# Optimization experiments

Measured on AMD Instinct MI355X. Metric: run time of the kernel, lower is better.

Reference implementation:

```python
import jax, jax.numpy as jnp
import numpy as np

EMBED_DIM = 1024
NUM_HEADS = 16
HEAD_DIM = EMBED_DIM // NUM_HEADS


def setup_inputs() -> dict:
    key = jax.random.key(0)
    ks = jax.random.split(key, 9)
    B, S, E, hd = 2, 2048, EMBED_DIM, HEAD_DIM
    s_e = 1.0 / np.sqrt(E)
    return {
        "x": jax.random.normal(ks[0], (B, S, E), dtype=jnp.float32),
        "wq": jax.random.uniform(ks[1], (E, E), jnp.float32, -s_e, s_e),
        "bq": jax.random.uniform(ks[2], (E,), jnp.float32, -s_e, s_e),
        "wk": jax.random.uniform(ks[3], (E, hd), jnp.float32, -s_e, s_e),
        "bk": jax.random.uniform(ks[4], (hd,), jnp.float32, -s_e, s_e),
        "wv": jax.random.uniform(ks[5], (E, hd), jnp.float32, -s_e, s_e),
        "bv": jax.random.uniform(ks[6], (hd,), jnp.float32, -s_e, s_e),
        "wo": jax.random.uniform(ks[7], (E, E), jnp.float32, -s_e, s_e),
        "bo": jax.random.uniform(ks[8], (E,), jnp.float32, -s_e, s_e),
    }


def reference(x, wq, bq, wk, bk, wv, bv, wo, bo):
    B, S, E = x.shape
    H, hd = NUM_HEADS, HEAD_DIM
    # projections
    q = (x @ wq + bq).reshape(B, S, H, hd)          # [B,S,H,hd]
    k = x @ wk + bk                                  # [B,S,hd] shared across heads
    v = x @ wv + bv                                  # [B,S,hd]
    scale = 1.0 / np.sqrt(hd).astype(np.float32)
    # scores: [B,H,S_q,S_k]
    scores = jnp.einsum('bqhd,bkd->bhqk', q, k) * scale
    attn = jax.nn.softmax(scores, axis=-1)
    out = jnp.einsum('bhqk,bkd->bqhd', attn, v).reshape(B, S, E)
    return out @ wo + bo
```

## Files before the change

kernel.cpp:

```cpp
#include <hip/hip_runtime.h>
#include <stdint.h>

#define SLEN 2048
#define EDIM 1024
#define NH 16
#define HD 64
#define QLD 1152
#define NSPLIT 2

typedef unsigned short u16;
typedef short bf8 __attribute__((ext_vector_type(8)));
typedef float f4 __attribute__((ext_vector_type(4)));
typedef float f16f __attribute__((ext_vector_type(16)));
typedef int v2i __attribute__((ext_vector_type(2)));
typedef bf8 bf8_a __attribute__((may_alias));
typedef uint2 uint2_a __attribute__((may_alias));
typedef uint4 uint4_a __attribute__((may_alias));

__device__ __forceinline__ float bf2f(u16 u) {
  union { unsigned u; float f; } c; c.u = ((unsigned)u) << 16; return c.f;
}
__device__ __forceinline__ u16 f2bf(float x) {
  union { __bf16 h; u16 u; } c; c.h = (__bf16)x; return c.u;
}
__device__ __forceinline__ unsigned pk2bf(float a, float b) {
  union { __bf16 h[2]; unsigned u; } c;
  c.h[0] = (__bf16)a; c.h[1] = (__bf16)b;
  return c.u;
}
__device__ __forceinline__ void async_cp16(u16* lds, const u16* g) {
  __builtin_amdgcn_global_load_lds((__attribute__((address_space(1))) void*)g,
                                   (__attribute__((address_space(3))) void*)lds,
                                   16, 0, 0);
}

__device__ __forceinline__ void tcvt_tile(const float* src, int srcLd,
                                          u16* dst, int dstLd, int r0, int c0) {
  __shared__ u16 tile[64][65];
  const int t = threadIdx.x;
#pragma unroll
  for (int i = 0; i < 16; ++i) {
    int e = i * 256 + t, rr = e >> 6, cc = e & 63;
    tile[rr][cc] = f2bf(src[(size_t)(r0 + rr) * srcLd + c0 + cc]);
  }
  __syncthreads();
#pragma unroll
  for (int i = 0; i < 16; ++i) {
    int e = i * 256 + t, j = e >> 6, ii = e & 63;
    dst[(size_t)(c0 + j) * dstLd + r0 + ii] = tile[ii][j];
  }
}

__global__ void prep_w(const float* wq, const float* wk, const float* wv,
                       const float* wo, const float* bq, const float* bk,
                       const float* bv, const float* bo, const float* x,
                       u16* wT, u16* woT, float* bQKV, float* bOut, u16* xbf) {
  const int yy = blockIdx.y;
  if (yy < 16) tcvt_tile(wq, 1024, wT, 1024, blockIdx.x * 64, yy * 64);
  else if (yy < 32) tcvt_tile(wo, 1024, woT, 1024, blockIdx.x * 64, (yy - 16) * 64);
  else if (yy == 32) tcvt_tile(wk, 64, wT + (size_t)1024 * 1024, 1024, blockIdx.x * 64, 0);
  else if (yy == 33) tcvt_tile(wv, 64, wT + (size_t)1088 * 1024, 1024, blockIdx.x * 64, 0);
  else if (yy == 34) {
    int i = blockIdx.x * 256 + threadIdx.x;
    if (i < 1024) bQKV[i] = bq[i];
    else if (i < 1088) bQKV[i] = bk[i - 1024];
    else if (i < 1152) bQKV[i] = bv[i - 1088];
    int j = i - 1152;
    if (j >= 0 && j < 1024) bOut[j] = bo[j];
  } else {
    const int blk = (yy - 35) * 16 + blockIdx.x, t = threadIdx.x;
#pragma unroll
    for (int i = 0; i < 8; ++i) {
      int idx = blk * 16384 + i * 2048 + t * 8;
      u16 tmp[8];
#pragma unroll
      for (int j = 0; j < 8; ++j) tmp[j] = f2bf(x[idx + j]);
      *(uint4_a*)&xbf[idx] = *(const uint4_a*)tmp;
    }
  }
}

__global__ __launch_bounds__(256) void gemm_bt_bias(
    const u16* __restrict__ A, const u16* __restrict__ Bt,
    const float* __restrict__ bias, void* __restrict__ C, int K, int ldc,
    int ofp32, u16* __restrict__ vtb) {
  __shared__ __align__(16) u16 As[64 * 64];
  __shared__ __align__(16) u16 Bs[128 * 64];
  const int tn0 = blockIdx.x * 128, tm0 = blockIdx.y * 64;
  const int tid = threadIdx.x, wave = tid >> 6, lane = tid & 63;
  const int quad = lane >> 4, l16 = lane & 15;
  const int wm = wave & 1, wn = wave >> 1;

  f4 acc[2][4];
#pragma unroll
  for (int i = 0; i < 2; ++i)
#pragma unroll
    for (int j = 0; j < 4; ++j) acc[i][j] = f4{0.f, 0.f, 0.f, 0.f};

  int aslot[2], bslot[4]; size_t aoff[2], boff[4];
#pragma unroll
  for (int i = 0; i < 2; ++i) {
    int s = i * 256 + tid, m = s >> 3, kc = s & 7, c = (kc - m) & 7;
    aslot[i] = s; aoff[i] = (size_t)(tm0 + m) * K + c * 8;
  }
#pragma unroll
  for (int i = 0; i < 4; ++i) {
    int s = i * 256 + tid, n = s >> 3, kc = s & 7, c = (kc - n) & 7;
    bslot[i] = s; boff[i] = (size_t)(tn0 + n) * K + c * 8;
  }
  int ard[2][2], brd[4][2];
#pragma unroll
  for (int mi = 0; mi < 2; ++mi) {
    int m = wm * 32 + mi * 16 + l16;
#pragma unroll
    for (int kk = 0; kk < 2; ++kk)
      ard[mi][kk] = (m * 8 + (((kk * 4 + quad) + m) & 7)) * 8;
  }
#pragma unroll
  for (int ni = 0; ni < 4; ++ni) {
    int n = wn * 64 + ni * 16 + l16;
#pragma unroll
    for (int kk = 0; kk < 2; ++kk)
      brd[ni][kk] = (n * 8 + (((kk * 4 + quad) + n) & 7)) * 8;
  }

  const int kIt = K >> 6;
  for (int it = 0; it < kIt; ++it) {
    __syncthreads();
    const size_t kb = (size_t)it * 64;
#pragma unroll
    for (int i = 0; i < 2; ++i) async_cp16(&As[aslot[i] * 8], A + aoff[i] + kb);
#pragma unroll
    for (int i = 0; i < 4; ++i) async_cp16(&Bs[bslot[i] * 8], Bt + boff[i] + kb);
    __syncthreads();
#pragma unroll
    for (int kk = 0; kk < 2; ++kk) {
      bf8 af[2], bfr[4];
#pragma unroll
      for (int mi = 0; mi < 2; ++mi) af[mi] = *(const bf8_a*)&As[ard[mi][kk]];
#pragma unroll
      for (int ni = 0; ni < 4; ++ni) bfr[ni] = *(const bf8_a*)&Bs[brd[ni][kk]];
#pragma unroll
      for (int mi = 0; mi < 2; ++mi)
#pragma unroll
        for (int ni = 0; ni < 4; ++ni)
          acc[mi][ni] = __builtin_amdgcn_mfma_f32_16x16x32_bf16(
              af[mi], bfr[ni], acc[mi][ni], 0, 0, 0);
    }
  }

  const float QSCALE = 0.125f * 1.44269504089f;
  float bv[4];
#pragma unroll
  for (int ni = 0; ni < 4; ++ni) bv[ni] = bias[tn0 + wn * 64 + ni * 16 + l16];
#pragma unroll
  for (int mi = 0; mi < 2; ++mi) {
    int row0 = tm0 + wm * 32 + mi * 16 + quad * 4;
#pragma unroll
    for (int ni = 0; ni < 4; ++ni) {
      int col = tn0 + wn * 64 + ni * 16 + l16;
      float vv[4];
#pragma unroll
      for (int r = 0; r < 4; ++r) vv[r] = acc[mi][ni][r] + bv[ni];
      if (vtb != nullptr && col < 1024) {
#pragma unroll
        for (int r = 0; r < 4; ++r) vv[r] *= QSCALE;
      }
      if (ofp32) {
#pragma unroll
        for (int r = 0; r < 4; ++r)
          ((float*)C)[(size_t)(row0 + r) * ldc + col] = vv[r];
      } else {
#pragma unroll
        for (int r = 0; r < 4; ++r)
          ((u16*)C)[(size_t)(row0 + r) * ldc + col] = f2bf(vv[r]);
      }
      if (vtb != nullptr && col >= 1088) {
        int d = col - 1088, bb = row0 >> 11, s0 = row0 & 2047;
        uint2 pk;
        pk.x = pk2bf(vv[0], vv[1]);
        pk.y = pk2bf(vv[2], vv[3]);
        *(uint2_a*)&vtb[(size_t)(bb * 64 + d) * SLEN + s0] = pk;
      }
    }
  }
}

__global__ __launch_bounds__(256, 4) void attn_kernel(
    const u16* __restrict__ qkv, const u16* __restrict__ vT,
    u16* __restrict__ Opart, float* __restrict__ lpart) {
  __shared__ __align__(16) u16 Kf[2][4096];
  __shared__ __align__(16) u16 Vf[2][4096];
  const int qt = blockIdx.x, bh = blockIdx.y, ks = blockIdx.z;
  const int b = bh >> 4, h = bh & 15;
  const int tid = threadIdx.x, wave = tid >> 6, lane = tid & 63;
  const int l31 = lane & 31, hi = lane >> 5, r16l = lane & 15;
  const int base_k = (l31 >> 4) * 64 + hi * 16 + r16l;

  u16* Kflat = &Kf[0][0];
#pragma unroll
  for (int i = 0; i < 4; ++i) {
    int d = i * 256 + tid;
    int kk = d >> 9, g = (d >> 6) & 7, qd = (d >> 4) & 3, r16 = d & 15;
    async_cp16(&Kflat[d * 8],
               qkv + (size_t)(b * SLEN + qt * 128 + g * 16 + r16) * QLD +
                   h * HD + (kk * 4 + qd) * 8);
  }
  __syncthreads();
  bf8 bq[4];
#pragma unroll
  for (int kk2 = 0; kk2 < 4; ++kk2) {
    int c = base_k + wave * 128 + (kk2 >> 1) * 512 + (kk2 & 1) * 32;
    bq[kk2] = *(const bf8_a*)&Kflat[c * 8];
  }
  __syncthreads();

  const int kbase = ks * (SLEN / NSPLIT);
  const u16* kp[2]; const u16* vp[2];
#pragma unroll
  for (int i = 0; i < 2; ++i) {
    int d = i * 256 + tid;
    int kk = d >> 8, k8 = (d >> 6) & 3, qd = (d >> 4) & 3, r16 = d & 15;
    kp[i] = qkv + (size_t)(b * SLEN + kbase + k8 * 16 + r16) * QLD + EDIM +
            (kk * 4 + qd) * 8;
    int k4 = d >> 8, ni = (d >> 6) & 3;
    vp[i] = vT + (size_t)(b * 64 + ni * 16 + r16) * SLEN + kbase +
            (k4 * 4 + qd) * 8;
  }
  auto stage = [&](int bsel) {
#pragma unroll
    for (int i = 0; i < 2; ++i) {
      int d = i * 256 + tid;
      async_cp16(&Kf[bsel][d * 8], kp[i]);
      async_cp16(&Vf[bsel][d * 8], vp[i]);
      kp[i] += 64 * QLD;
      vp[i] += 64;
    }
  };
  stage(0);

  f16f acc_o[2];
#pragma unroll
  for (int i = 0; i < 2; ++i)
#pragma unroll
    for (int r = 0; r < 16; ++r) acc_o[i][r] = 0.f;
  f4 lracc = f4{0.f, 0.f, 0.f, 0.f};

  const int NHALF = SLEN / NSPLIT / 64;
  for (int hh = 0; hh < NHALF; ++hh) {
    __syncthreads();
    if (hh < NHALF - 1) stage((hh + 1) & 1);
    const int bsel = hh & 1;
    const u16* kf = &Kf[bsel][0];
    const u16* vf = &Vf[bsel][0];

    f16f st[2];
#pragma unroll
    for (int j = 0; j < 2; ++j)
#pragma unroll
      for (int r = 0; r < 16; ++r) st[j][r] = 0.f;
    __builtin_amdgcn_s_setprio(1);
#pragma unroll
    for (int kk2 = 0; kk2 < 4; ++kk2) {
#pragma unroll
      for (int j32 = 0; j32 < 2; ++j32) {
        bf8 ak = *(const bf8_a*)
            &kf[(base_k + (kk2 >> 1) * 256 + j32 * 128 + (kk2 & 1) * 32) * 8];
        st[j32] = __builtin_amdgcn_mfma_f32_32x32x16_bf16(ak, bq[kk2],
                                                          st[j32], 0, 0, 0);
      }
    }
    __builtin_amdgcn_s_setprio(0);

    bf8 pa[2][2];
#pragma unroll
    for (int j32 = 0; j32 < 2; ++j32) {
      float pe[16];
#pragma unroll
      for (int r = 0; r < 16; ++r) {
        pe[r] = __builtin_amdgcn_exp2f(st[j32][r]);
        lracc[r & 3] += pe[r];
      }
      int a0 = (int)pk2bf(pe[0], pe[1]),   b0 = (int)pk2bf(pe[4], pe[5]);
      int a1 = (int)pk2bf(pe[2], pe[3]),   b1 = (int)pk2bf(pe[6], pe[7]);
      int a2 = (int)pk2bf(pe[8], pe[9]),   b2 = (int)pk2bf(pe[12], pe[13]);
      int a3 = (int)pk2bf(pe[10], pe[11]), b3 = (int)pk2bf(pe[14], pe[15]);
      v2i s0 = __builtin_amdgcn_permlane32_swap(a0, b0, false, false);
      v2i s1 = __builtin_amdgcn_permlane32_swap(a1, b1, false, false);
      v2i s2 = __builtin_amdgcn_permlane32_swap(a2, b2, false, false);
      v2i s3 = __builtin_amdgcn_permlane32_swap(a3, b3, false, false);
      union { int i[4]; bf8 v; } up0, up1;
      up0.i[0] = s0[0]; up0.i[1] = s1[0]; up0.i[2] = s0[1]; up0.i[3] = s1[1];
      up1.i[0] = s2[0]; up1.i[1] = s3[0]; up1.i[2] = s2[1]; up1.i[3] = s3[1];
      pa[j32][0] = up0.v;
      pa[j32][1] = up1.v;
    }

    __builtin_amdgcn_s_setprio(1);
#pragma unroll
    for (int j32 = 0; j32 < 2; ++j32)
#pragma unroll
      for (int ks2 = 0; ks2 < 2; ++ks2)
#pragma unroll
        for (int ni2 = 0; ni2 < 2; ++ni2) {
          bf8 bv = *(const bf8_a*)
              &vf[(base_k + j32 * 256 + ni2 * 128 + ks2 * 32) * 8];
          acc_o[ni2] = __builtin_amdgcn_mfma_f32_32x32x16_bf16(
              pa[j32][ks2], bv, acc_o[ni2], 0, 0, 0);
        }
    __builtin_amdgcn_s_setprio(0);
  }

  const size_t pbase = (size_t)((ks * 32 + bh) * 16 + qt) * 128;
  float lr = (lracc[0] + lracc[1]) + (lracc[2] + lracc[3]);
  float s = lr + __shfl_xor(lr, 32, 64);
  if (lane < 32) lpart[pbase + wave * 32 + lane] = s;
#pragma unroll
  for (int ni2 = 0; ni2 < 2; ++ni2)
#pragma unroll
    for (int r = 0; r < 16; ++r) {
      int q = (r & 3) + 8 * (r >> 2) + 4 * hi;
      Opart[(pbase + wave * 32 + q) * 64 + ni2 * 32 + l31] =
          f2bf(acc_o[ni2][r]);
    }
}

__global__ __launch_bounds__(256) void reduce_o(const u16* __restrict__ Op,
                                                const float* __restrict__ lp,
                                                u16* __restrict__ aob) {
  const int qt = blockIdx.x, bh = blockIdx.y, b = bh >> 4, h = bh & 15;
  const int t = threadIdx.x, r = t >> 1, dh = (t & 1) * 32;
  size_t p[NSPLIT];
#pragma unroll
  for (int i = 0; i < NSPLIT; ++i)
    p[i] = (size_t)((i * 32 + bh) * 16 + qt) * 128;
  float lsum = 0.f;
#pragma unroll
  for (int i = 0; i < NSPLIT; ++i) lsum += lp[p[i] + r];
  const float inv = 1.f / lsum;
  u16* dst = aob + (size_t)(b * SLEN + qt * 128 + r) * EDIM + h * HD + dh;
#pragma unroll
  for (int c = 0; c < 4; ++c) {
    float accv[8] = {0.f, 0.f, 0.f, 0.f, 0.f, 0.f, 0.f, 0.f};
#pragma unroll
    for (int i = 0; i < NSPLIT; ++i) {
      uint4 a = *(const uint4_a*)(Op + (p[i] + r) * 64 + dh + c * 8);
      const u16* pa = (const u16*)&a;
#pragma unroll
      for (int j = 0; j < 8; ++j) accv[j] += bf2f(pa[j]);
    }
    u16 outv[8];
#pragma unroll
    for (int j = 0; j < 8; ++j) outv[j] = f2bf(accv[j] * inv);
    *(uint4_a*)(dst + c * 8) = *(const uint4_a*)outv;
  }
}

extern "C" void kernel_launch(void* const* d_in, const int* in_sizes, int n_in,
                              void* d_out, int out_size, void* d_ws, size_t ws_size,
                              hipStream_t stream) {
  const float* x  = (const float*)d_in[0];
  const float* wq = (const float*)d_in[1];
  const float* bq = (const float*)d_in[2];
  const float* wk = (const float*)d_in[3];
  const float* bk = (const float*)d_in[4];
  const float* wv = (const float*)d_in[5];
  const float* bv = (const float*)d_in[6];
  const float* wo = (const float*)d_in[7];
  const float* bo = (const float*)d_in[8];

  char* ws = (char*)d_ws;
  size_t off = 0;
  auto carve = [&](size_t bytes) {
    void* p = ws + off;
    off = (off + bytes + 255) & ~(size_t)255;
    return p;
  };
  u16* wT      = (u16*)carve((size_t)1152 * 1024 * 2);
  u16* woT     = (u16*)carve((size_t)1024 * 1024 * 2);
  float* bQKV  = (float*)carve(1152 * 4);
  float* bOut  = (float*)carve(1024 * 4);
  u16* xbf     = (u16*)carve((size_t)4096 * EDIM * 2);
  u16* qkvb    = (u16*)carve((size_t)4096 * QLD * 2);
  u16* vTb     = (u16*)carve((size_t)2 * 64 * SLEN * 2);
  u16* Opart   = (u16*)carve((size_t)NSPLIT * 32 * 16 * 128 * 64 * 2);
  float* lpart = (float*)carve((size_t)NSPLIT * 32 * 16 * 128 * 4);
  u16* aob     = (u16*)carve((size_t)4096 * EDIM * 2);

  prep_w<<<dim3(16, 51), 256, 0, stream>>>(wq, wk, wv, wo, bq, bk, bv, bo, x,
                                           wT, woT, bQKV, bOut, xbf);

  gemm_bt_bias<<<dim3(9, 64), 256, 0, stream>>>(xbf, wT, bQKV, qkvb, 1024, QLD,
                                                0, vTb);

  attn_kernel<<<dim3(16, 32, NSPLIT), 256, 0, stream>>>(qkvb, vTb, Opart, lpart);
  reduce_o<<<dim3(16, 32), 256, 0, stream>>>(Opart, lpart, aob);

  gemm_bt_bias<<<dim3(8, 64), 256, 0, stream>>>(aob, woT, bOut, d_out, 1024,
                                                1024, 1, nullptr);
}
```

Baseline: 182.3 us.

## Process 256 query rows per attention block to reuse K/V tiles

Each attention block now handles 256 queries instead of 128, with each wave holding two 32-query sets. Every K and V tile staged in shared memory is reused across twice as many MFMAs, which halves the K/V global and LDS traffic per query. In exchange the block uses roughly double the accumulator registers (launch bounds drop from 4 to 2 waves-per-SIMD hint) and the grid is half as many blocks (512 total), which may reduce occupancy and latency hiding. The reduce kernel indexing is updated to match the new partial layout.

Measured after the change: 178.1 us. 1.02x faster.

```diff
diff --git a/kernel.cpp b/kernel.cpp
--- a/kernel.cpp
+++ b/kernel.cpp
@@ -186,7 +186,7 @@
   }
 }
 
-__global__ __launch_bounds__(256, 4) void attn_kernel(
+__global__ __launch_bounds__(256, 2) void attn_kernel(
     const u16* __restrict__ qkv, const u16* __restrict__ vT,
     u16* __restrict__ Opart, float* __restrict__ lpart) {
   __shared__ __align__(16) u16 Kf[2][4096];
@@ -198,20 +198,30 @@
   const int base_k = (l31 >> 4) * 64 + hi * 16 + r16l;
 
   u16* Kflat = &Kf[0][0];
-#pragma unroll
-  for (int i = 0; i < 4; ++i) {
+  u16* Vflat = &Vf[0][0];
+#pragma unroll
+  for (int i = 0; i < 8; ++i) {
     int d = i * 256 + tid;
-    int kk = d >> 9, g = (d >> 6) & 7, qd = (d >> 4) & 3, r16 = d & 15;
-    async_cp16(&Kflat[d * 8],
-               qkv + (size_t)(b * SLEN + qt * 128 + g * 16 + r16) * QLD +
+    int sel = d >> 10, dl = d & 1023;
+    int kk = dl >> 9, g = (dl >> 6) & 7, qd = (dl >> 4) & 3, r16 = dl & 15;
+    u16* dstf = sel ? Vflat : Kflat;
+    async_cp16(&dstf[dl * 8],
+               qkv + (size_t)(b * SLEN + qt * 256 + sel * 128 + g * 16 + r16) * QLD +
                    h * HD + (kk * 4 + qd) * 8);
   }
   __syncthreads();
-  bf8 bq[4];
-#pragma unroll
-  for (int kk2 = 0; kk2 < 4; ++kk2) {
-    int c = base_k + wave * 128 + (kk2 >> 1) * 512 + (kk2 & 1) * 32;
-    bq[kk2] = *(const bf8_a*)&Kflat[c * 8];
+  bf8 bq[2][4];
+  {
+    const u16* srcf = (wave >> 1) ? Vflat : Kflat;
+#pragma unroll
+    for (int qset = 0; qset < 2; ++qset) {
+      int gq = (wave & 1) * 2 + qset;
+#pragma unroll
+      for (int kk2 = 0; kk2 < 4; ++kk2) {
+        int c = base_k + gq * 128 + (kk2 >> 1) * 512 + (kk2 & 1) * 32;
+        bq[qset][kk2] = *(const bf8_a*)&srcf[c * 8];
+      }
+    }
   }
   __syncthreads();
 
@@ -239,12 +249,14 @@
   };
   stage(0);
 
-  f16f acc_o[2];
-#pragma unroll
-  for (int i = 0; i < 2; ++i)
-#pragma unroll
-    for (int r = 0; r < 16; ++r) acc_o[i][r] = 0.f;
-  f4 lracc = f4{0.f, 0.f, 0.f, 0.f};
+  f16f acc_o[2][2];
+#pragma unroll
+  for (int qset = 0; qset < 2; ++qset)
+#pragma unroll
+    for (int i = 0; i < 2; ++i)
+#pragma unroll
+      for (int r = 0; r < 16; ++r) acc_o[qset][i][r] = 0.f;
+  f4 lracc[2] = {f4{0.f, 0.f, 0.f, 0.f}, f4{0.f, 0.f, 0.f, 0.f}};
 
   const int NHALF = SLEN / NSPLIT / 64;
   for (int hh = 0; hh < NHALF; ++hh) {
@@ -254,75 +266,78 @@
     const u16* kf = &Kf[bsel][0];
     const u16* vf = &Vf[bsel][0];
 
-    f16f st[2];
-#pragma unroll
-    for (int j = 0; j < 2; ++j)
-#pragma unroll
-      for (int r = 0; r < 16; ++r) st[j][r] = 0.f;
-    __builtin_amdgcn_s_setprio(1);
-#pragma unroll
-    for (int kk2 = 0; kk2 < 4; ++kk2) {
-#pragma unroll
-      for (int j32 = 0; j32 < 2; ++j32) {
+#pragma unroll
+    for (int j32 = 0; j32 < 2; ++j32) {
+      f16f st0, st1;
+#pragma unroll
+      for (int r = 0; r < 16; ++r) { st0[r] = 0.f; st1[r] = 0.f; }
+      __builtin_amdgcn_s_setprio(1);
+#pragma unroll
+      for (int kk2 = 0; kk2 < 4; ++kk2) {
         bf8 ak = *(const bf8_a*)
             &kf[(base_k + (kk2 >> 1) * 256 + j32 * 128 + (kk2 & 1) * 32) * 8];
-        st[j32] = __builtin_amdgcn_mfma_f32_32x32x16_bf16(ak, bq[kk2],
-                                                          st[j32], 0, 0, 0);
-      }
-    }
-    __builtin_amdgcn_s_setprio(0);
-
-    bf8 pa[2][2];
-#pragma unroll
-    for (int j32 = 0; j32 < 2; ++j32) {
-      float pe[16];
-#pragma unroll
-      for (int r = 0; r < 16; ++r) {
-        pe[r] = __builtin_amdgcn_exp2f(st[j32][r]);
-        lracc[r & 3] += pe[r];
-      }
-      int a0 = (int)pk2bf(pe[0], pe[1]),   b0 = (int)pk2bf(pe[4], pe[5]);
-      int a1 = (int)pk2bf(pe[2], pe[3]),   b1 = (int)pk2bf(pe[6], pe[7]);
-      int a2 = (int)pk2bf(pe[8], pe[9]),   b2 = (int)pk2bf(pe[12], pe[13]);
-      int a3 = (int)pk2bf(pe[10], pe[11]), b3 = (int)pk2bf(pe[14], pe[15]);
-      v2i s0 = __builtin_amdgcn_permlane32_swap(a0, b0, false, false);
-      v2i s1 = __builtin_amdgcn_permlane32_swap(a1, b1, false, false);
-      v2i s2 = __builtin_amdgcn_permlane32_swap(a2, b2, false, false);
-      v2i s3 = __builtin_amdgcn_permlane32_swap(a3, b3, false, false);
-      union { int i[4]; bf8 v; } up0, up1;
-      up0.i[0] = s0[0]; up0.i[1] = s1[0]; up0.i[2] = s0[1]; up0.i[3] = s1[1];
-      up1.i[0] = s2[0]; up1.i[1] = s3[0]; up1.i[2] = s2[1]; up1.i[3] = s3[1];
-      pa[j32][0] = up0.v;
-      pa[j32][1] = up1.v;
-    }
-
-    __builtin_amdgcn_s_setprio(1);
-#pragma unroll
-    for (int j32 = 0; j32 < 2; ++j32)
+        st0 = __builtin_amdgcn_mfma_f32_32x32x16_bf16(ak, bq[0][kk2], st0, 0, 0, 0);
+        st1 = __builtin_amdgcn_mfma_f32_32x32x16_bf16(ak, bq[1][kk2], st1, 0, 0, 0);
+      }
+      __builtin_amdgcn_s_setprio(0);
+
+      bf8 pa[2][2];
+#pragma unroll
+      for (int qset = 0; qset < 2; ++qset) {
+        float pe[16];
+#pragma unroll
+        for (int r = 0; r < 16; ++r) {
+          pe[r] = __builtin_amdgcn_exp2f(qset ? st1[r] : st0[r]);
+          lracc[qset][r & 3] += pe[r];
+        }
+        int a0 = (int)pk2bf(pe[0], pe[1]),   b0 = (int)pk2bf(pe[4], pe[5]);
+        int a1 = (int)pk2bf(pe[2], pe[3]),   b1 = (int)pk2bf(pe[6], pe[7]);
+        int a2 = (int)pk2bf(pe[8], pe[9]),   b2 = (int)pk2bf(pe[12], pe[13]);
+        int a3 = (int)pk2bf(pe[10], pe[11]), b3 = (int)pk2bf(pe[14], pe[15]);
+        v2i s0 = __builtin_amdgcn_permlane32_swap(a0, b0, false, false);
+        v2i s1 = __builtin_amdgcn_permlane32_swap(a1, b1, false, false);
+        v2i s2 = __builtin_amdgcn_permlane32_swap(a2, b2, false, false);
+        v2i s3 = __builtin_amdgcn_permlane32_swap(a3, b3, false, false);
+        union { int i[4]; bf8 v; } up0, up1;
+        up0.i[0] = s0[0]; up0.i[1] = s1[0]; up0.i[2] = s0[1]; up0.i[3] = s1[1];
+        up1.i[0] = s2[0]; up1.i[1] = s3[0]; up1.i[2] = s2[1]; up1.i[3] = s3[1];
+        pa[qset][0] = up0.v;
+        pa[qset][1] = up1.v;
+      }
+
+      __builtin_amdgcn_s_setprio(1);
 #pragma unroll
       for (int ks2 = 0; ks2 < 2; ++ks2)
 #pragma unroll
         for (int ni2 = 0; ni2 < 2; ++ni2) {
           bf8 bv = *(const bf8_a*)
               &vf[(base_k + j32 * 256 + ni2 * 128 + ks2 * 32) * 8];
-          acc_o[ni2] = __builtin_amdgcn_mfma_f32_32x32x16_bf16(
-              pa[j32][ks2], bv, acc_o[ni2], 0, 0, 0);
+          acc_o[0][ni2] = __builtin_amdgcn_mfma_f32_32x32x16_bf16(
+              pa[0][ks2], bv, acc_o[0][ni2], 0, 0, 0);
+          acc_o[1][ni2] = __builtin_amdgcn_mfma_f32_32x32x16_bf16(
+              pa[1][ks2], bv, acc_o[1][ni2], 0, 0, 0);
         }
-    __builtin_amdgcn_s_setprio(0);
-  }
-
-  const size_t pbase = (size_t)((ks * 32 + bh) * 16 + qt) * 128;
-  float lr = (lracc[0] + lracc[1]) + (lracc[2] + lracc[3]);
-  float s = lr + __shfl_xor(lr, 32, 64);
-  if (lane < 32) lpart[pbase + wave * 32 + lane] = s;
-#pragma unroll
-  for (int ni2 = 0; ni2 < 2; ++ni2)
-#pragma unroll
-    for (int r = 0; r < 16; ++r) {
-      int q = (r & 3) + 8 * (r >> 2) + 4 * hi;
-      Opart[(pbase + wave * 32 + q) * 64 + ni2 * 32 + l31] =
-          f2bf(acc_o[ni2][r]);
-    }
+      __builtin_amdgcn_s_setprio(0);
+    }
+  }
+
+  const size_t pbase = (size_t)((ks * 32 + bh) * 8 + qt) * 256;
+#pragma unroll
+  for (int qset = 0; qset < 2; ++qset) {
+    float lr = (lracc[qset][0] + lracc[qset][1]) + (lracc[qset][2] + lracc[qset][3]);
+    float s = lr + __shfl_xor(lr, 32, 64);
+    if (lane < 32) lpart[pbase + wave * 64 + qset * 32 + lane] = s;
+  }
+#pragma unroll
+  for (int qset = 0; qset < 2; ++qset)
+#pragma unroll
+    for (int ni2 = 0; ni2 < 2; ++ni2)
+#pragma unroll
+      for (int r = 0; r < 16; ++r) {
+        int q = (r & 3) + 8 * (r >> 2) + 4 * hi;
+        Opart[(pbase + wave * 64 + qset * 32 + q) * 64 + ni2 * 32 + l31] =
+            f2bf(acc_o[qset][ni2][r]);
+      }
 }
 
 __global__ __launch_bounds__(256) void reduce_o(const u16* __restrict__ Op,
@@ -330,21 +345,23 @@
                                                 u16* __restrict__ aob) {
   const int qt = blockIdx.x, bh = blockIdx.y, b = bh >> 4, h = bh & 15;
   const int t = threadIdx.x, r = t >> 1, dh = (t & 1) * 32;
+  const int g = qt * 128 + r;
+  const int blk = g >> 8, loc = g & 255;
   size_t p[NSPLIT];
 #pragma unroll
   for (int i = 0; i < NSPLIT; ++i)
-    p[i] = (size_t)((i * 32 + bh) * 16 + qt) * 128;
+    p[i] = (size_t)((i * 32 + bh) * 8 + blk) * 256 + loc;
   float lsum = 0.f;
 #pragma unroll
-  for (int i = 0; i < NSPLIT; ++i) lsum += lp[p[i] + r];
+  for (int i = 0; i < NSPLIT; ++i) lsum += lp[p[i]];
   const float inv = 1.f / lsum;
-  u16* dst = aob + (size_t)(b * SLEN + qt * 128 + r) * EDIM + h * HD + dh;
+  u16* dst = aob + (size_t)(b * SLEN + g) * EDIM + h * HD + dh;
 #pragma unroll
   for (int c = 0; c < 4; ++c) {
     float accv[8] = {0.f, 0.f, 0.f, 0.f, 0.f, 0.f, 0.f, 0.f};
 #pragma unroll
     for (int i = 0; i < NSPLIT; ++i) {
-      uint4 a = *(const uint4_a*)(Op + (p[i] + r) * 64 + dh + c * 8);
+      uint4 a = *(const uint4_a*)(Op + p[i] * 64 + dh + c * 8);
       const u16* pa = (const u16*)&a;
 #pragma unroll
       for (int j = 0; j < 8; ++j) accv[j] += bf2f(pa[j]);
@@ -383,8 +400,8 @@
   u16* xbf     = (u16*)carve((size_t)4096 * EDIM * 2);
   u16* qkvb    = (u16*)carve((size_t)4096 * QLD * 2);
   u16* vTb     = (u16*)carve((size_t)2 * 64 * SLEN * 2);
-  u16* Opart   = (u16*)carve((size_t)NSPLIT * 32 * 16 * 128 * 64 * 2);
-  float* lpart = (float*)carve((size_t)NSPLIT * 32 * 16 * 128 * 4);
+  u16* Opart   = (u16*)carve((size_t)NSPLIT * 32 * 8 * 256 * 64 * 2);
+  float* lpart = (float*)carve((size_t)NSPLIT * 32 * 8 * 256 * 4);
   u16* aob     = (u16*)carve((size_t)4096 * EDIM * 2);
 
   prep_w<<<dim3(16, 51), 256, 0, stream>>>(wq, wk, wv, wo, bq, bk, bv, bo, x,
@@ -393,7 +410,7 @@
   gemm_bt_bias<<<dim3(9, 64), 256, 0, stream>>>(xbf, wT, bQKV, qkvb, 1024, QLD,
                                                 0, vTb);
 
-  attn_kernel<<<dim3(16, 32, NSPLIT), 256, 0, stream>>>(qkvb, vTb, Opart, lpart);
+  attn_kernel<<<dim3(8, 32, NSPLIT), 256, 0, stream>>>(qkvb, vTb, Opart, lpart);
   reduce_o<<<dim3(16, 32), 256, 0, stream>>>(Opart, lpart, aob);
 
   gemm_bt_bias<<<dim3(8, 64), 256, 0, stream>>>(aob, woT, bOut, d_out, 1024,
```
